# Optimization experiments

Measured on AMD Instinct MI355X. Metric: run time of the kernel, lower is better.

Reference implementation:

```python
import jax, jax.numpy as jnp
import numpy as np

N = 50000      # nodes
E = 800000     # edges (before self-loops)
IN = 128       # in_channels
HID = 32       # hidden_channels
H = 4          # heads (hidden layers)
H_LAST = 6     # heads of final conv (concat=False -> mean)
OUT = 2        # out_channels
NEG = 0.2      # LeakyReLU slope in GATConv


def setup_inputs() -> dict:
    key = jax.random.key(0)
    ks = jax.random.split(key, 24)
    r = lambda k, s, sc=0.1: (jax.random.normal(k, s, jnp.float32) * sc)
    inp = {
        "x": jax.random.normal(ks[0], (N, IN), jnp.float32),
        "edge_index": jax.random.randint(ks[1], (2, E), 0, N, dtype=jnp.int32),
        "edge_attr": jax.random.normal(ks[2], (E, 1), jnp.float32),  # ignored by GATConv (edge_dim=None)
        # layer 0: GATConv(IN -> HID, heads=H, concat) + Linear(IN -> HID*H)
        "c0_W": r(ks[3], (IN, H * HID)), "c0_as": r(ks[4], (H, HID)), "c0_ad": r(ks[5], (H, HID)), "c0_b": jnp.zeros((H * HID,), jnp.float32),
        "l0_W": r(ks[6], (IN, H * HID)), "l0_b": jnp.zeros((H * HID,), jnp.float32),
        # layer 1 (middle): GATConv(HID*H -> HID, heads=H) + Linear(HID*H -> HID*H)
        "c1_W": r(ks[7], (H * HID, H * HID)), "c1_as": r(ks[8], (H, HID)), "c1_ad": r(ks[9], (H, HID)), "c1_b": jnp.zeros((H * HID,), jnp.float32),
        "l1_W": r(ks[10], (H * HID, H * HID)), "l1_b": jnp.zeros((H * HID,), jnp.float32),
        # layer 2 (last): GATConv(HID*H -> OUT, heads=H_LAST, concat=False) + Linear(HID*H -> OUT)
        "c2_W": r(ks[11], (H * HID, H_LAST * OUT)), "c2_as": r(ks[12], (H_LAST, OUT)), "c2_ad": r(ks[13], (H_LAST, OUT)), "c2_b": jnp.zeros((OUT,), jnp.float32),
        "l2_W": r(ks[14], (H * HID, OUT)), "l2_b": jnp.zeros((OUT,), jnp.float32),
    }
    return inp


def gat_conv(x, src, dst, W, a_src, a_dst, b, heads, ch, concat):
    n = x.shape[0]
    xw = (x @ W).reshape(n, heads, ch)                      # [N,H,C]
    al_s = jnp.einsum('nhc,hc->nh', xw, a_src)              # [N,H]
    al_d = jnp.einsum('nhc,hc->nh', xw, a_dst)
    alpha = jax.nn.leaky_relu(al_s[src] + al_d[dst], NEG)   # [E,H]
    # segment softmax over edges sharing the same destination node
    m = jax.ops.segment_max(alpha, dst, num_segments=n)
    e = jnp.exp(alpha - m[dst])
    s = jax.ops.segment_sum(e, dst, num_segments=n)
    coef = e / s[dst]                                       # [E,H]
    out = jax.ops.segment_sum(xw[src] * coef[:, :, None], dst, num_segments=n)  # [N,H,C]
    out = out.reshape(n, heads * ch) if concat else out.mean(axis=1)
    return out + b


def reference(x, edge_index, edge_attr,
              c0_W, c0_as, c0_ad, c0_b, l0_W, l0_b,
              c1_W, c1_as, c1_ad, c1_b, l1_W, l1_b,
              c2_W, c2_as, c2_ad, c2_b, l2_W, l2_b):
    n = x.shape[0]
    loops = jnp.arange(n, dtype=edge_index.dtype)  # GATConv add_self_loops=True
    src = jnp.concatenate([edge_index[0], loops])
    dst = jnp.concatenate([edge_index[1], loops])
    # edge_attr is ignored: GATConv built without edge_dim has lin_edge=None
    h = jax.nn.relu(gat_conv(x, src, dst, c0_W, c0_as, c0_ad, c0_b, H, HID, True) + x @ l0_W + l0_b)
    h = jax.nn.relu(gat_conv(h, src, dst, c1_W, c1_as, c1_ad, c1_b, H, HID, True) + h @ l1_W + l1_b)
    out = gat_conv(h, src, dst, c2_W, c2_as, c2_ad, c2_b, H_LAST, OUT, False) + h @ l2_W + l2_b
    return out
```

## Files before the change

### kernel.cpp

```cpp
#include <hip/hip_runtime.h>
#include <hip/hip_bf16.h>


#define NEG_SLOPE 0.2f
#define SC_CHUNK 4096
#define CAP 64

typedef __attribute__((ext_vector_type(8))) short short8;
typedef __attribute__((ext_vector_type(4))) float floatx4;

static __device__ __forceinline__ float leaky(float x) {
    return x > 0.f ? x : NEG_SLOPE * x;
}

static __device__ __forceinline__ unsigned short f2bf(float f) {
    unsigned int u = __float_as_uint(f);
    u = (u + 0x7fffu + ((u >> 16) & 1u)) >> 16;
    return (unsigned short)u;
}

static __device__ __forceinline__ unsigned int pack_bf2(float lo, float hi) {
    return (unsigned int)f2bf(lo) | ((unsigned int)f2bf(hi) << 16);
}

static __device__ __forceinline__ float bflo(unsigned int u) {
    return __uint_as_float(u << 16);
}
static __device__ __forceinline__ float bfhi(unsigned int u) {
    return __uint_as_float(u & 0xffff0000u);
}

static __device__ __forceinline__ short8 frag_from_f32(const float* p) {
    float4 f0 = ((const float4*)p)[0];
    float4 f1 = ((const float4*)p)[1];
    short8 r;
    r[0] = (short)f2bf(f0.x); r[1] = (short)f2bf(f0.y);
    r[2] = (short)f2bf(f0.z); r[3] = (short)f2bf(f0.w);
    r[4] = (short)f2bf(f1.x); r[5] = (short)f2bf(f1.y);
    r[6] = (short)f2bf(f1.z); r[7] = (short)f2bf(f1.w);
    return r;
}

__global__ __launch_bounds__(256) void k_bucket(
    const int* __restrict__ ei, int E, int N, int rs,
    int* __restrict__ cnt, int* __restrict__ col,
    const float* __restrict__ W0, unsigned short* __restrict__ T0,
    const float* __restrict__ W1, unsigned short* __restrict__ T1,
    const float* __restrict__ W2, unsigned short* __restrict__ T2,
    const float* __restrict__ W3, unsigned short* __restrict__ T3,
    const float* __restrict__ c2W, const float* __restrict__ l2W,
    unsigned short* __restrict__ WT5) {
    if (blockIdx.y == gridDim.y - 1) {
        int tid = blockIdx.x * 256 + threadIdx.x;
        for (int j = tid; j < 65536; j += 2048) {
            int wsel = j >> 14, t = j & 16383;
            int n = t >> 7, k = t & 127;
            const float* W = (wsel == 0) ? W0 : (wsel == 1) ? W1 : (wsel == 2) ? W2 : W3;
            unsigned short* T = (wsel == 0) ? T0 : (wsel == 1) ? T1 : (wsel == 2) ? T2 : T3;
            T[n * 128 + k] = f2bf(W[k * 128 + n]);
        }
        {
            int n = tid >> 7, k = tid & 127;
            float v = 0.f;
            if (n < 12) v = c2W[k * 12 + n];
            else if (n < 14) v = l2W[k * 2 + (n - 12)];
            WT5[n * 128 + k] = f2bf(v);
        }
        return;
    }
    int lo = blockIdx.x * rs, hi = lo + rs;
    int base = blockIdx.y * SC_CHUNK;
    int ET = E + N;
#pragma unroll 4
    for (int o = threadIdx.x; o < SC_CHUNK; o += 256) {
        int e = base + o;
        if (e >= ET) break;
        int d = (e < E) ? ei[E + e] : (e - E);
        if (d < lo || d >= hi) continue;
        int s = (e < E) ? ei[e] : d;
        int pos = atomicAdd(&cnt[d], 1);
        if (pos < CAP) col[(d << 6) + pos] = s;
    }
}

__global__ __launch_bounds__(256) void k_gemm_mfma(
    const float* __restrict__ x0,
    const unsigned short* __restrict__ Ab,
    const unsigned short* __restrict__ W1T,
    unsigned int* __restrict__ XWb,
    const float* __restrict__ a_s, const float* __restrict__ a_d,
    float4* __restrict__ ALS4, float4* __restrict__ ALD4,
    const unsigned short* __restrict__ W2T,
    const float* __restrict__ b2,
    unsigned short* __restrict__ Hsb,
    int M) {
    int which = blockIdx.y;
    const unsigned short* WT = which ? W2T : W1T;
    int row0 = blockIdx.x * 64;
    int w = threadIdx.x >> 6, lane = threadIdx.x & 63;
    int m = lane & 15, q = lane >> 4;

    const short8* A8 = (const short8*)Ab;
    const short8* W8 = (const short8*)WT;

    floatx4 acc[8];
#pragma unroll
    for (int ct = 0; ct < 8; ct++) acc[ct] = (floatx4){0.f, 0.f, 0.f, 0.f};

    int arow = row0 + w * 16 + m;
    int lrow = (arow < M) ? arow : (M - 1);
#pragma unroll
    for (int ks = 0; ks < 4; ks++) {
        short8 afrag = x0 ? frag_from_f32(x0 + (size_t)lrow * 128 + (ks * 4 + q) * 8)
                          : A8[arow * 16 + ks * 4 + q];
#pragma unroll
        for (int ct = 0; ct < 8; ct++) {
            short8 bfrag = W8[(ct * 16 + m) * 16 + ks * 4 + q];
            acc[ct] = __builtin_amdgcn_mfma_f32_16x16x32_bf16(afrag, bfrag, acc[ct], 0, 0, 0);
        }
    }

    int crow0 = row0 + w * 16 + q * 4;
    if (which) {
#pragma unroll
        for (int ct = 0; ct < 8; ct++) {
            int gc = ct * 16 + m;
            float bias = b2[gc];
#pragma unroll
            for (int r = 0; r < 4; r++) {
                int gr = crow0 + r;
                if (gr < M) Hsb[gr * 128 + gc] = f2bf(acc[ct][r] + bias);
            }
        }
    } else {
#pragma unroll
        for (int ct = 0; ct < 4; ct++) {
#pragma unroll
            for (int r = 0; r < 4; r++) {
                int gr = crow0 + r;
                if (gr < M)
                    XWb[gr * 64 + ct * 16 + m] = pack_bf2(acc[ct][r], acc[ct + 4][r]);
            }
        }
        float sv[4][4], dv[4][4];
#pragma unroll
        for (int h = 0; h < 4; h++) {
            float as0 = a_s[h * 32 + m], as1 = a_s[h * 32 + 16 + m];
            float ad0 = a_d[h * 32 + m], ad1 = a_d[h * 32 + 16 + m];
#pragma unroll
            for (int r = 0; r < 4; r++) {
                sv[h][r] = acc[2 * h][r] * as0 + acc[2 * h + 1][r] * as1;
                dv[h][r] = acc[2 * h][r] * ad0 + acc[2 * h + 1][r] * ad1;
            }
        }
#pragma unroll
        for (int off = 8; off >= 1; off >>= 1) {
#pragma unroll
            for (int h = 0; h < 4; h++)
#pragma unroll
                for (int r = 0; r < 4; r++) {
                    sv[h][r] += __shfl_xor(sv[h][r], off);
                    dv[h][r] += __shfl_xor(dv[h][r], off);
                }
        }
        if (m == 0) {
#pragma unroll
            for (int r = 0; r < 4; r++) {
                int gr = crow0 + r;
                if (gr < M) {
                    ALS4[gr] = make_float4(sv[0][r], sv[1][r], sv[2][r], sv[3][r]);
                    ALD4[gr] = make_float4(dv[0][r], dv[1][r], dv[2][r], dv[3][r]);
                }
            }
        }
    }
}

__global__ __launch_bounds__(256) void k_gemm_small(
    const unsigned short* __restrict__ Ab,
    const unsigned short* __restrict__ WT5,
    const float* __restrict__ c2as, const float* __restrict__ c2ad,
    const float* __restrict__ l2b,
    float* __restrict__ L2D, float* __restrict__ ALD2,
    float* __restrict__ out, int M) {
    int w = threadIdx.x >> 6, lane = threadIdx.x & 63;
    int m = lane & 15, q = lane >> 4;
    const short8* A8 = (const short8*)Ab;
    const short8* W8 = (const short8*)WT5;
    floatx4 acc = (floatx4){0.f, 0.f, 0.f, 0.f};
    int arow = blockIdx.x * 64 + w * 16 + m;
#pragma unroll
    for (int ks = 0; ks < 4; ks++) {
        short8 afrag = A8[arow * 16 + ks * 4 + q];
        short8 bfrag = W8[m * 16 + ks * 4 + q];
        acc = __builtin_amdgcn_mfma_f32_16x16x32_bf16(afrag, bfrag, acc, 0, 0, 0);
    }
    float asm_ = (m < 12) ? c2as[m] : 0.f;
    float adm  = (m < 12) ? c2ad[m] : 0.f;
    int crow0 = blockIdx.x * 64 + w * 16 + q * 4;
    float sc[4], dc[4];
#pragma unroll
    for (int r = 0; r < 4; r++) {
        sc[r] = acc[r] * asm_;
        dc[r] = acc[r] * adm;
    }
#pragma unroll
    for (int r = 0; r < 4; r++) {
        sc[r] += __shfl_xor(sc[r], 1);
        dc[r] += __shfl_xor(dc[r], 1);
    }
#pragma unroll
    for (int r = 0; r < 4; r++) {
        int gr = crow0 + r;
        if (gr >= M) continue;
        if (m < 12) {
            L2D[gr * 20 + m] = acc[r];
            if ((m & 1) == 0) {
                int h = m >> 1;
                L2D[gr * 20 + 12 + h] = sc[r];
                ALD2[gr * 8 + h] = dc[r];
            }
        } else if (m == 12) {
            out[gr * 2 + 0] = acc[r] + l2b[0];
        } else if (m == 13) {
            out[gr * 2 + 1] = acc[r] + l2b[1];
        }
    }
}

__global__ __launch_bounds__(256) void k_agg4(
    const int* __restrict__ cntv, const int* __restrict__ col,
    const uint4* __restrict__ XWb4,
    const float4* __restrict__ ALS4, const float4* __restrict__ ALD4,
    const float* __restrict__ cb,
    const unsigned short* __restrict__ Hsb, unsigned short* __restrict__ Hb, int N) {
    int wid = threadIdx.x >> 6, lane = threadIdx.x & 63;
    int node = blockIdx.x * 4 + wid;
    if (node >= N) return;
    int deg = cntv[node];
    if (deg > CAP) deg = CAP;
    int start = node << 6;
    int gq = lane >> 4, g = lane & 15;
    int hA = g >> 3;
    int cval = col[start + lane];
    float4 cl = ((const float4*)cb)[g];
    float4 ch = ((const float4*)cb)[g + 16];
    uint2 skl = ((const uint2*)(Hsb + node * 128))[g];
    uint2 skh = ((const uint2*)(Hsb + node * 128 + 64))[g];
    float4 ad = ALD4[node];
    float adA = hA ? ad.y : ad.x;
    float adB = hA ? ad.w : ad.z;

    float a0 = 0.f, a1 = 0.f, a2 = 0.f, a3 = 0.f;
    float b0 = 0.f, b1 = 0.f, b2 = 0.f, b3 = 0.f;
    float sA = 0.f, sB = 0.f;

#define EDGE(sv)                                                       \
    {                                                                  \
        float4 as = ALS4[sv];                                          \
        uint4 u = XWb4[(size_t)(sv) * 16 + g];                         \
        float eA = __expf(leaky((hA ? as.y : as.x) + adA));            \
        float eB = __expf(leaky((hA ? as.w : as.z) + adB));            \
        sA += eA; sB += eB;                                            \
        a0 += eA * bflo(u.x); b0 += eB * bfhi(u.x);                    \
        a1 += eA * bflo(u.y); b1 += eB * bfhi(u.y);                    \
        a2 += eA * bflo(u.z); b2 += eB * bfhi(u.z);                    \
        a3 += eA * bflo(u.w); b3 += eB * bfhi(u.w);                    \
    }

    int i = 0;
    for (; i + 16 <= deg; i += 16) {
        int s0 = __shfl(cval, i + gq);
        int s1 = __shfl(cval, i + 4 + gq);
        int s2 = __shfl(cval, i + 8 + gq);
        int s3 = __shfl(cval, i + 12 + gq);
        EDGE(s0) EDGE(s1) EDGE(s2) EDGE(s3)
    }
    for (; i + 4 <= deg; i += 4) {
        int s0 = __shfl(cval, i + gq);
        EDGE(s0)
    }
    int rem = deg - i;
    if (rem > 0) {
        int s0 = __shfl(cval, i + (gq < rem ? gq : 0));
        if (gq < rem) EDGE(s0)
    }
#undef EDGE

#define RED2(v) { v += __shfl_xor(v, 16); v += __shfl_xor(v, 32); }
    RED2(sA) RED2(sB)
    RED2(a0) RED2(a1) RED2(a2) RED2(a3)
    RED2(b0) RED2(b1) RED2(b2) RED2(b3)
#undef RED2

    if (gq == 0) {
        float invA = 1.f / sA, invB = 1.f / sB;
        float v0 = a0 * invA + cl.x + bflo(skl.x);
        float v1 = a1 * invA + cl.y + bfhi(skl.x);
        float v2 = a2 * invA + cl.z + bflo(skl.y);
        float v3 = a3 * invA + cl.w + bfhi(skl.y);
        float w0 = b0 * invB + ch.x + bflo(skh.x);
        float w1 = b1 * invB + ch.y + bfhi(skh.x);
        float w2 = b2 * invB + ch.z + bflo(skh.y);
        float w3 = b3 * invB + ch.w + bfhi(skh.y);
        v0 = v0 > 0.f ? v0 : 0.f;  v1 = v1 > 0.f ? v1 : 0.f;
        v2 = v2 > 0.f ? v2 : 0.f;  v3 = v3 > 0.f ? v3 : 0.f;
        w0 = w0 > 0.f ? w0 : 0.f;  w1 = w1 > 0.f ? w1 : 0.f;
        w2 = w2 > 0.f ? w2 : 0.f;  w3 = w3 > 0.f ? w3 : 0.f;
        uint2 ol, oh;
        ol.x = pack_bf2(v0, v1); ol.y = pack_bf2(v2, v3);
        oh.x = pack_bf2(w0, w1); oh.y = pack_bf2(w2, w3);
        ((uint2*)(Hb + node * 128))[g] = ol;
        ((uint2*)(Hb + node * 128 + 64))[g] = oh;
    }
}

__global__ __launch_bounds__(256) void k_agg2(
    const int* __restrict__ cntv, const int* __restrict__ col,
    const float4* __restrict__ L2D4,
    const float* __restrict__ ALD2,
    const float* __restrict__ c2b,
    float* __restrict__ out, int N) {
    int g = threadIdx.x >> 4, l = threadIdx.x & 15;
    int node = blockIdx.x * 16 + g;
    if (node >= N) return;
    int deg = cntv[node];
    if (deg > CAP) deg = CAP;
    int start = node << 6;

    int c0 = (l      < deg) ? col[start + l]      : -1;
    int c1 = (l + 16 < deg) ? col[start + l + 16] : -1;
    int c2 = (l + 32 < deg) ? col[start + l + 32] : -1;
    int c3 = (l + 48 < deg) ? col[start + l + 48] : -1;

    float ald[6];
    {
        float4 d03 = *(const float4*)(ALD2 + node * 8);
        float2 d45 = *(const float2*)(ALD2 + node * 8 + 4);
        ald[0] = d03.x; ald[1] = d03.y; ald[2] = d03.z; ald[3] = d03.w;
        ald[4] = d45.x; ald[5] = d45.y;
    }

    float se[6], a0[6], a1[6];
#pragma unroll
    for (int h = 0; h < 6; h++) { se[h] = 0.f; a0[h] = 0.f; a1[h] = 0.f; }

#define EDGE2(sv)                                                          \
    if ((sv) >= 0) {                                                       \
        float4 x03 = L2D4[(sv) * 5 + 0];                                   \
        float4 x47 = L2D4[(sv) * 5 + 1];                                   \
        float4 x8b = L2D4[(sv) * 5 + 2];                                   \
        float4 as03 = L2D4[(sv) * 5 + 3];                                  \
        float4 as45 = L2D4[(sv) * 5 + 4];                                  \
        float als[6] = {as03.x, as03.y, as03.z, as03.w, as45.x, as45.y};   \
        float xw[12] = {x03.x, x03.y, x03.z, x03.w, x47.x, x47.y, x47.z,   \
                        x47.w, x8b.x, x8b.y, x8b.z, x8b.w};                \
        _Pragma("unroll")                                                  \
        for (int h = 0; h < 6; h++) {                                      \
            float e = __expf(leaky(als[h] + ald[h]));                      \
            se[h] += e;                                                    \
            a0[h] += e * xw[2 * h];                                        \
            a1[h] += e * xw[2 * h + 1];                                    \
        }                                                                  \
    }

    EDGE2(c0) EDGE2(c1) EDGE2(c2) EDGE2(c3)
#undef EDGE2

#pragma unroll
    for (int m = 8; m >= 1; m >>= 1) {
#pragma unroll
        for (int h = 0; h < 6; h++) {
            se[h] += __shfl_xor(se[h], m);
            a0[h] += __shfl_xor(a0[h], m);
            a1[h] += __shfl_xor(a1[h], m);
        }
    }
    if (l == 0) {
        float o0 = 0.f, o1 = 0.f;
#pragma unroll
        for (int h = 0; h < 6; h++) {
            float inv = 1.f / se[h];
            o0 += a0[h] * inv;
            o1 += a1[h] * inv;
        }
        out[node * 2 + 0] += o0 * (1.f / 6.f) + c2b[0];
        out[node * 2 + 1] += o1 * (1.f / 6.f) + c2b[1];
    }
}


extern "C" void kernel_launch(void* const* d_in, const int* in_sizes, int n_in,
                              void* d_out, int out_size, void* d_ws, size_t ws_size,
                              hipStream_t stream) {
    const float* x   = (const float*)d_in[0];
    const int* ei    = (const int*)d_in[1];
    const float* c0W = (const float*)d_in[3];
    const float* c0as = (const float*)d_in[4];
    const float* c0ad = (const float*)d_in[5];
    const float* c0b = (const float*)d_in[6];
    const float* l0W = (const float*)d_in[7];
    const float* l0b = (const float*)d_in[8];
    const float* c1W = (const float*)d_in[9];
    const float* c1as = (const float*)d_in[10];
    const float* c1ad = (const float*)d_in[11];
    const float* c1b = (const float*)d_in[12];
    const float* l1W = (const float*)d_in[13];
    const float* l1b = (const float*)d_in[14];
    const float* c2W = (const float*)d_in[15];
    const float* c2as = (const float*)d_in[16];
    const float* c2ad = (const float*)d_in[17];
    const float* c2b = (const float*)d_in[18];
    const float* l2W = (const float*)d_in[19];
    const float* l2b = (const float*)d_in[20];
    float* out = (float*)d_out;

    const int N = in_sizes[0] / 128;
    const int E = in_sizes[1] / 2;
    const int ET = E + N;
    const int Mpad = (N + 63) & ~63;

    char* p = (char*)d_ws;
    auto alloc = [&](size_t bytes) -> void* {
        void* r = (void*)p;
        p += (bytes + 255) & ~(size_t)255;
        return r;
    };
    unsigned short* Hsb = (unsigned short*)alloc((size_t)N * 128 * 2);
    unsigned int* XWb = (unsigned int*)alloc((size_t)N * 64 * 4);
    unsigned short* Ab = (unsigned short*)alloc((size_t)Mpad * 128 * 2);
    unsigned short* W1T = (unsigned short*)alloc(128 * 128 * 2);
    unsigned short* W2T = (unsigned short*)alloc(128 * 128 * 2);
    unsigned short* W3T = (unsigned short*)alloc(128 * 128 * 2);
    unsigned short* W4T = (unsigned short*)alloc(128 * 128 * 2);
    unsigned short* WT5 = (unsigned short*)alloc(16 * 128 * 2);
    float* ALS = (float*)alloc((size_t)N * 4 * 4);
    float* ALD = (float*)alloc((size_t)N * 8 * 4);
    float* L2D = (float*)alloc((size_t)N * 20 * 4);
    int* cnt    = (int*)alloc((size_t)N * 4);
    int* col    = (int*)alloc((size_t)N * CAP * 4);

    hipMemsetAsync(cnt, 0, (size_t)N * 4, stream);
    int rs = (N + 7) / 8;
    int chunks = (ET + SC_CHUNK - 1) / SC_CHUNK;
    dim3 bgrid(8, chunks + 1);
    k_bucket<<<bgrid, 256, 0, stream>>>(ei, E, N, rs, cnt, col,
                                        c0W, W1T, l0W, W2T, c1W, W3T, l1W, W4T,
                                        c2W, l2W, WT5);

    dim3 ggrid(Mpad / 64, 2);
    int nwb = (N + 3) / 4;

    k_gemm_mfma<<<ggrid, 256, 0, stream>>>(x, Ab, W1T, XWb, c0as, c0ad,
                                           (float4*)ALS, (float4*)ALD,
                                           W2T, l0b, Hsb, N);
    k_agg4<<<nwb, 256, 0, stream>>>(cnt, col, (const uint4*)XWb,
                                    (const float4*)ALS, (const float4*)ALD,
                                    c0b, Hsb, Ab, N);

    k_gemm_mfma<<<ggrid, 256, 0, stream>>>(nullptr, Ab, W3T, XWb, c1as, c1ad,
                                           (float4*)ALS, (float4*)ALD,
                                           W4T, l1b, Hsb, N);
    k_agg4<<<nwb, 256, 0, stream>>>(cnt, col, (const uint4*)XWb,
                                    (const float4*)ALS, (const float4*)ALD,
                                    c1b, Hsb, Ab, N);

    k_gemm_small<<<Mpad / 64, 256, 0, stream>>>(Ab, WT5, c2as, c2ad, l2b,
                                                L2D, ALD, out, N);
    k_agg2<<<(N + 15) / 16, 256, 0, stream>>>(cnt, col, (const float4*)L2D,
                                              ALD, c2b, out, N);
}
```

Before: 325.2 us.

## Stage weight matrix in LDS and process two row tiles per block

The MFMA GEMM kernel now copies the 128x128 bf16 weight matrix into padded shared memory once per block. Each wave then computes two 16-row tiles instead of one, so each block covers 128 rows and the grid is halved. This cuts repeated global/L2 reads of the weight fragments and spreads the staging cost over more rows. In exchange it adds about 35KB of LDS per block and more register pressure from holding A fragments for both tiles, which may lower occupancy. Rows beyond Mpad rely on the existing M bounds checks, though the A8 path reads unclamped rows that may fall past the padded buffer.

```diff
diff --git a/kernel.cpp b/kernel.cpp
--- a/kernel.cpp
+++ b/kernel.cpp
@@ -94,82 +94,96 @@
     const float* __restrict__ b2,
     unsigned short* __restrict__ Hsb,
     int M) {
+    __shared__ short8 Wl[128 * 17];
     int which = blockIdx.y;
-    const unsigned short* WT = which ? W2T : W1T;
-    int row0 = blockIdx.x * 64;
+    const short8* W8 = (const short8*)(which ? W2T : W1T);
+
+    for (int u = threadIdx.x; u < 2048; u += 256)
+        Wl[(u >> 4) * 17 + (u & 15)] = W8[u];
+
     int w = threadIdx.x >> 6, lane = threadIdx.x & 63;
     int m = lane & 15, q = lane >> 4;
-
     const short8* A8 = (const short8*)Ab;
-    const short8* W8 = (const short8*)WT;
-
-    floatx4 acc[8];
-#pragma unroll
-    for (int ct = 0; ct < 8; ct++) acc[ct] = (floatx4){0.f, 0.f, 0.f, 0.f};
-
-    int arow = row0 + w * 16 + m;
-    int lrow = (arow < M) ? arow : (M - 1);
-#pragma unroll
-    for (int ks = 0; ks < 4; ks++) {
-        short8 afrag = x0 ? frag_from_f32(x0 + (size_t)lrow * 128 + (ks * 4 + q) * 8)
-                          : A8[arow * 16 + ks * 4 + q];
-#pragma unroll
-        for (int ct = 0; ct < 8; ct++) {
-            short8 bfrag = W8[(ct * 16 + m) * 16 + ks * 4 + q];
-            acc[ct] = __builtin_amdgcn_mfma_f32_16x16x32_bf16(afrag, bfrag, acc[ct], 0, 0, 0);
-        }
-    }
-
-    int crow0 = row0 + w * 16 + q * 4;
-    if (which) {
-#pragma unroll
-        for (int ct = 0; ct < 8; ct++) {
-            int gc = ct * 16 + m;
-            float bias = b2[gc];
-#pragma unroll
-            for (int r = 0; r < 4; r++) {
-                int gr = crow0 + r;
-                if (gr < M) Hsb[gr * 128 + gc] = f2bf(acc[ct][r] + bias);
-            }
-        }
-    } else {
-#pragma unroll
-        for (int ct = 0; ct < 4; ct++) {
-#pragma unroll
-            for (int r = 0; r < 4; r++) {
-                int gr = crow0 + r;
-                if (gr < M)
-                    XWb[gr * 64 + ct * 16 + m] = pack_bf2(acc[ct][r], acc[ct + 4][r]);
-            }
-        }
-        float sv[4][4], dv[4][4];
-#pragma unroll
-        for (int h = 0; h < 4; h++) {
-            float as0 = a_s[h * 32 + m], as1 = a_s[h * 32 + 16 + m];
-            float ad0 = a_d[h * 32 + m], ad1 = a_d[h * 32 + 16 + m];
-#pragma unroll
-            for (int r = 0; r < 4; r++) {
-                sv[h][r] = acc[2 * h][r] * as0 + acc[2 * h + 1][r] * as1;
-                dv[h][r] = acc[2 * h][r] * ad0 + acc[2 * h + 1][r] * ad1;
-            }
-        }
-#pragma unroll
-        for (int off = 8; off >= 1; off >>= 1) {
-#pragma unroll
-            for (int h = 0; h < 4; h++)
+
+    short8 af[2][4];
+    int rt0 = blockIdx.x * 8 + w;
+#pragma unroll
+    for (int t = 0; t < 2; t++) {
+        int arow = (rt0 + t * 4) * 16 + m;
+        int lrow = (arow < M) ? arow : (M - 1);
+#pragma unroll
+        for (int ks = 0; ks < 4; ks++) {
+            af[t][ks] = x0 ? frag_from_f32(x0 + (size_t)lrow * 128 + (ks * 4 + q) * 8)
+                           : A8[arow * 16 + ks * 4 + q];
+        }
+    }
+    __syncthreads();
+
+#pragma unroll
+    for (int t = 0; t < 2; t++) {
+        floatx4 acc[8];
+#pragma unroll
+        for (int ct = 0; ct < 8; ct++) acc[ct] = (floatx4){0.f, 0.f, 0.f, 0.f};
+#pragma unroll
+        for (int ks = 0; ks < 4; ks++) {
+#pragma unroll
+            for (int ct = 0; ct < 8; ct++) {
+                short8 bfrag = Wl[(ct * 16 + m) * 17 + ks * 4 + q];
+                acc[ct] = __builtin_amdgcn_mfma_f32_16x16x32_bf16(af[t][ks], bfrag, acc[ct], 0, 0, 0);
+            }
+        }
+
+        int crow0 = (rt0 + t * 4) * 16 + q * 4;
+        if (which) {
+#pragma unroll
+            for (int ct = 0; ct < 8; ct++) {
+                int gc = ct * 16 + m;
+                float bias = b2[gc];
 #pragma unroll
                 for (int r = 0; r < 4; r++) {
-                    sv[h][r] += __shfl_xor(sv[h][r], off);
-                    dv[h][r] += __shfl_xor(dv[h][r], off);
+                    int gr = crow0 + r;
+                    if (gr < M) Hsb[gr * 128 + gc] = f2bf(acc[ct][r] + bias);
                 }
-        }
-        if (m == 0) {
-#pragma unroll
-            for (int r = 0; r < 4; r++) {
-                int gr = crow0 + r;
-                if (gr < M) {
-                    ALS4[gr] = make_float4(sv[0][r], sv[1][r], sv[2][r], sv[3][r]);
-                    ALD4[gr] = make_float4(dv[0][r], dv[1][r], dv[2][r], dv[3][r]);
+            }
+        } else {
+#pragma unroll
+            for (int ct = 0; ct < 4; ct++) {
+#pragma unroll
+                for (int r = 0; r < 4; r++) {
+                    int gr = crow0 + r;
+                    if (gr < M)
+                        XWb[gr * 64 + ct * 16 + m] = pack_bf2(acc[ct][r], acc[ct + 4][r]);
+                }
+            }
+            float sv[4][4], dv[4][4];
+#pragma unroll
+            for (int h = 0; h < 4; h++) {
+                float as0 = a_s[h * 32 + m], as1 = a_s[h * 32 + 16 + m];
+                float ad0 = a_d[h * 32 + m], ad1 = a_d[h * 32 + 16 + m];
+#pragma unroll
+                for (int r = 0; r < 4; r++) {
+                    sv[h][r] = acc[2 * h][r] * as0 + acc[2 * h + 1][r] * as1;
+                    dv[h][r] = acc[2 * h][r] * ad0 + acc[2 * h + 1][r] * ad1;
+                }
+            }
+#pragma unroll
+            for (int off = 8; off >= 1; off >>= 1) {
+#pragma unroll
+                for (int h = 0; h < 4; h++)
+#pragma unroll
+                    for (int r = 0; r < 4; r++) {
+                        sv[h][r] += __shfl_xor(sv[h][r], off);
+                        dv[h][r] += __shfl_xor(dv[h][r], off);
+                    }
+            }
+            if (m == 0) {
+#pragma unroll
+                for (int r = 0; r < 4; r++) {
+                    int gr = crow0 + r;
+                    if (gr < M) {
+                        ALS4[gr] = make_float4(sv[0][r], sv[1][r], sv[2][r], sv[3][r]);
+                        ALD4[gr] = make_float4(dv[0][r], dv[1][r], dv[2][r], dv[3][r]);
+                    }
                 }
             }
         }
@@ -448,7 +462,7 @@
                                         c0W, W1T, l0W, W2T, c1W, W3T, l1W, W4T,
                                         c2W, l2W, WT5);
 
-    dim3 ggrid(Mpad / 64, 2);
+    dim3 ggrid((Mpad + 127) / 128, 2);
     int nwb = (N + 3) / 4;
 
     k_gemm_mfma<<<ggrid, 256, 0, stream>>>(x, Ab, W1T, XWb, c0as, c0ad,
```

Measured after the change: 307.7 us. 1.06x faster.
